# Performance work log

Measured on AMD Instinct MI355X. Metric: run time of the kernel, lower is better.

The kernel has to match this reference:

```python
import jax, jax.numpy as jnp
import numpy as np
import math

N_HEAD = 16

def _c(a):
    # stack real/imag -> complex64
    return jax.lax.complex(a[..., 0], a[..., 1])

def _rope_phasor(T, D, dtype=jnp.float32):
    inv_freq = 1.0 / (10000.0 ** (jnp.arange(D, dtype=dtype) / D))
    t = jnp.arange(T, dtype=dtype)
    freqs = jnp.outer(t, inv_freq)  # [T, D]
    return jax.lax.complex(jnp.cos(freqs), jnp.sin(freqs))

def setup_inputs() -> dict:
    key = jax.random.key(0)
    ks = jax.random.split(key, 9)
    B, T, C = 2, 1024, 1024
    s = 0.02
    return {
        "x":  jax.random.normal(ks[0], (B, T, C, 2), jnp.float32),
        "wq": jax.random.normal(ks[1], (C, C, 2), jnp.float32) * s,
        "bq": jax.random.normal(ks[2], (C, 2), jnp.float32) * s,
        "wk": jax.random.normal(ks[3], (C, C, 2), jnp.float32) * s,
        "bk": jax.random.normal(ks[4], (C, 2), jnp.float32) * s,
        "wv": jax.random.normal(ks[5], (C, C, 2), jnp.float32) * s,
        "bv": jax.random.normal(ks[6], (C, 2), jnp.float32) * s,
        "wo": jax.random.normal(ks[7], (C, C, 2), jnp.float32) * s,
        "bo": jax.random.normal(ks[8], (C, 2), jnp.float32) * s,
    }

def reference(x, wq, bq, wk, bk, wv, bv, wo, bo):
    B, T, C, _ = x.shape
    H = N_HEAD
    D = C // H
    xc = _c(x)
    # complex linear projections: y = x @ W^T + b
    q = xc @ _c(wq).T + _c(bq)
    k = xc @ _c(wk).T + _c(bk)
    v = xc @ _c(wv).T + _c(bv)
    # [B, T, C] -> [B, H, T, D]
    q = q.reshape(B, T, H, D).transpose(0, 2, 1, 3)
    k = k.reshape(B, T, H, D).transpose(0, 2, 1, 3)
    v = v.reshape(B, T, H, D).transpose(0, 2, 1, 3)
    # complex RoPE phasor multiply
    ph = _rope_phasor(T, D)[None, None]  # [1,1,T,D]
    q = q * ph
    k = k * ph
    # complex QK^H, scaled
    score = jnp.einsum('bhtd,bhsd->bhts', q, jnp.conj(k)) / math.sqrt(D)
    # softmax over magnitude, then real-valued complex weights
    attn = jax.nn.softmax(jnp.abs(score), axis=-1)
    attn_c = jax.lax.complex(attn, jnp.zeros_like(attn))
    out = jnp.einsum('bhts,bhsd->bhtd', attn_c, v)
    out = out.transpose(0, 2, 1, 3).reshape(B, T, C)
    out = out @ _c(wo).T + _c(bo)
    # return real/imag stacked for a real-valued harness
    return jnp.stack([out.real, out.imag], axis=-1)
```

## Files before the change

### kernel.cpp

```cpp
#include <hip/hip_runtime.h>
#include <math.h>

#define T_SEQ  1024
#define C_DIM  1024
#define NH_    16
#define H_DIM  64
#define SCL    (0.125f * 1.4426950408889634f)

typedef __bf16 bf16;
typedef __bf16 bf16x4 __attribute__((ext_vector_type(4)));
typedef __bf16 bf16x8 __attribute__((ext_vector_type(8)));
typedef float  f32x4  __attribute__((ext_vector_type(4)));

#define MFMA16(a, b, c) __builtin_amdgcn_mfma_f32_16x16x32_bf16(a, b, c, 0, 0, 0)

#define GLOAD_LDS16(g, l) __builtin_amdgcn_global_load_lds( \
    (const __attribute__((address_space(1))) void*)(g),     \
    (__attribute__((address_space(3))) void*)(l), 16, 0, 0)

__device__ __forceinline__ bf16x8 neg8(bf16x8 x) {
    union { bf16x8 v; unsigned int u[4]; } t;
    t.v = x;
    t.u[0] ^= 0x80008000u; t.u[1] ^= 0x80008000u;
    t.u[2] ^= 0x80008000u; t.u[3] ^= 0x80008000u;
    return t.v;
}

__device__ __forceinline__ bf16x8 frag_sw(const bf16* plane, int row, int chunk) {
    int c = chunk ^ (row & 7);
    return *(const bf16x8*)&plane[row * 64 + c * 8];
}
__device__ __forceinline__ bf16x8 frag_sw4(const bf16* plane, int row, int chunk) {
    int c = chunk ^ (row & 3);
    return *(const bf16x8*)&plane[row * 32 + c * 8];
}

__global__ __launch_bounds__(256)
void split_all(const float* __restrict__ x,  const float* __restrict__ wq,
               const float* __restrict__ wk, const float* __restrict__ wv,
               const float* __restrict__ wo,
               bf16* Xr, bf16* Xi, bf16* Wqr, bf16* Wqi, bf16* Wkr, bf16* Wki,
               bf16* Wvr, bf16* Wvi, bf16* Wor, bf16* Woi,
               float* __restrict__ rope)
{
    int z = blockIdx.y;
    if (z == 5) {
        if (blockIdx.x >= 256) return;
        int idx = blockIdx.x * 256 + threadIdx.x;
        int tp = idx >> 6, d = idx & 63;
        float invf = exp2f((float)d * -0.2076205059304601f);
        float fr = (float)tp * invf;
        float sn, cs; sincosf(fr, &sn, &cs);
        *(float2*)&rope[(size_t)idx * 2] = make_float2(cs, sn);
        return;
    }
    if (z > 0 && blockIdx.x >= 1024) return;
    const float* in; bf16 *pr, *pi;
    if      (z == 0) { in = x;  pr = Xr;  pi = Xi;  }
    else if (z == 1) { in = wq; pr = Wqr; pi = Wqi; }
    else if (z == 2) { in = wk; pr = Wkr; pi = Wki; }
    else if (z == 3) { in = wv; pr = Wvr; pi = Wvi; }
    else             { in = wo; pr = Wor; pi = Woi; }
    int idx = (blockIdx.x * 256 + threadIdx.x) * 4;
    float4 v0 = *(const float4*)(in + (size_t)idx * 2);
    float4 v1 = *(const float4*)(in + (size_t)idx * 2 + 4);
    bf16x4 r, im;
    r[0] = (bf16)v0.x; r[1] = (bf16)v0.z; r[2] = (bf16)v1.x; r[3] = (bf16)v1.z;
    im[0] = (bf16)v0.y; im[1] = (bf16)v0.w; im[2] = (bf16)v1.y; im[3] = (bf16)v1.w;
    *(bf16x4*)(pr + idx) = r;
    *(bf16x4*)(pi + idx) = im;
}

__device__ __forceinline__ void cgemm128(
    bf16* __restrict__ smem,
    const bf16* __restrict__ Ar, const bf16* __restrict__ Ai,
    const bf16* __restrict__ Br, const bf16* __restrict__ Bi,
    const float* __restrict__ bias, const float* __restrict__ rope,
    bf16* __restrict__ Yr, bf16* __restrict__ Yi, int m0, int n0, int mode)
{
    const int t = threadIdx.x, lane = t & 63, wave = t >> 6;
    const int wm = (wave >> 1) * 64, wn = (wave & 1) * 32;
    const int lm = lane & 15, quad = lane >> 4;
    const int s_lr = lane >> 3, s_c = (lane & 7) ^ s_lr;

    f32x4 accr[4][2], acci[4][2];
#pragma unroll
    for (int i = 0; i < 4; i++)
#pragma unroll
        for (int j = 0; j < 2; j++) { accr[i][j] = (f32x4)0.f; acci[i][j] = (f32x4)0.f; }

    for (int k0 = 0; k0 < C_DIM; k0 += 64) {
#pragma unroll
        for (int j = 0; j < 12; j++) {
            int c = wave + 4 * j;
            const bf16* src; bf16* dst;
            if (c < 16)      {             src = Ar + (size_t)(m0 + c * 8 + s_lr) * C_DIM + k0 + s_c * 8; dst = smem + c * 512; }
            else if (c < 32) { int u = c - 16; src = Ai + (size_t)(m0 + u * 8 + s_lr) * C_DIM + k0 + s_c * 8; dst = smem + 8192 + u * 512; }
            else if (c < 40) { int u = c - 32; src = Br + (size_t)(n0 + u * 8 + s_lr) * C_DIM + k0 + s_c * 8; dst = smem + 16384 + u * 512; }
            else             { int u = c - 40; src = Bi + (size_t)(n0 + u * 8 + s_lr) * C_DIM + k0 + s_c * 8; dst = smem + 20480 + u * 512; }
            GLOAD_LDS16(src, dst);
        }
        __syncthreads();

#pragma unroll
        for (int kh = 0; kh < 2; kh++) {
            bf16x8 ar[4], ai_[4], br_[2], bi_[2], bn_[2];
#pragma unroll
            for (int i = 0; i < 4; i++) {
                ar[i]  = frag_sw(smem,        wm + i * 16 + lm, kh * 4 + quad);
                ai_[i] = frag_sw(smem + 8192, wm + i * 16 + lm, kh * 4 + quad);
            }
#pragma unroll
            for (int j = 0; j < 2; j++) {
                br_[j] = frag_sw(smem + 16384, wn + j * 16 + lm, kh * 4 + quad);
                bi_[j] = frag_sw(smem + 20480, wn + j * 16 + lm, kh * 4 + quad);
                bn_[j] = neg8(bi_[j]);
            }
#pragma unroll
            for (int i = 0; i < 4; i++)
#pragma unroll
                for (int j = 0; j < 2; j++) {
                    accr[i][j] = MFMA16(ar[i],  br_[j], accr[i][j]);
                    accr[i][j] = MFMA16(ai_[i], bn_[j], accr[i][j]);
                    acci[i][j] = MFMA16(ar[i],  bi_[j], acci[i][j]);
                    acci[i][j] = MFMA16(ai_[i], br_[j], acci[i][j]);
                }
        }
        __syncthreads();
    }

    const int h = n0 >> 6, bb = m0 >> 10, tbase = m0 & (T_SEQ - 1);

    if (mode == 1) {
#pragma unroll
        for (int i = 0; i < 4; i++)
#pragma unroll
            for (int j = 0; j < 2; j++) {
                int d = wn + j * 16 + lm;
                float2 bv = *(const float2*)&bias[2 * (n0 + d)];
#pragma unroll
                for (int r = 0; r < 4; r++) {
                    int tpos = tbase + wm + i * 16 + quad * 4 + r;
                    float2 ph = *(const float2*)&rope[((size_t)tpos * H_DIM + d) * 2];
                    float yr = accr[i][j][r] + bv.x;
                    float yi = acci[i][j][r] + bv.y;
                    accr[i][j][r] = yr * ph.x - yi * ph.y;
                    acci[i][j][r] = yr * ph.y + yi * ph.x;
                }
            }
        bf16* dsts[2] = { Yr, Yi };
#pragma unroll
        for (int pass = 0; pass < 2; pass++) {
            __syncthreads();
#pragma unroll
            for (int i = 0; i < 4; i++)
#pragma unroll
                for (int j = 0; j < 2; j++)
#pragma unroll
                    for (int r = 0; r < 4; r++)
                        smem[(wm + i * 16 + quad * 4 + r) * 72 + wn + j * 16 + lm] =
                            (bf16)(pass ? acci[i][j][r] : accr[i][j][r]);
            __syncthreads();
            bf16* dst = dsts[pass] + ((size_t)(bb * NH_ + h) * T_SEQ + tbase) * H_DIM;
#pragma unroll
            for (int p = 0; p < 4; p++) {
                int ch = t + 256 * p;
                int row = ch >> 3, o = (ch & 7) * 8;
                *(bf16x8*)&dst[row * H_DIM + o] = *(const bf16x8*)&smem[row * 72 + o];
            }
        }
    } else {
        bf16* dsts[2] = { Yr, Yi };
#pragma unroll
        for (int pass = 0; pass < 2; pass++) {
            __syncthreads();
#pragma unroll
            for (int i = 0; i < 4; i++)
#pragma unroll
                for (int j = 0; j < 2; j++) {
                    int d = wn + j * 16 + lm;
                    float2 bv = *(const float2*)&bias[2 * (n0 + d)];
                    float bb2 = pass ? bv.y : bv.x;
                    bf16x4 pk;
#pragma unroll
                    for (int r = 0; r < 4; r++)
                        pk[r] = (bf16)((pass ? acci[i][j][r] : accr[i][j][r]) + bb2);
                    *(bf16x4*)&smem[d * 136 + wm + i * 16 + quad * 4] = pk;
                }
            __syncthreads();
            bf16* dst = dsts[pass] + ((size_t)(bb * NH_ + h) * H_DIM) * T_SEQ + tbase;
#pragma unroll
            for (int p = 0; p < 4; p++) {
                int ch = t + 256 * p;
                int row = ch >> 4, o = (ch & 15) * 8;
                *(bf16x8*)&dst[(size_t)row * T_SEQ + o] = *(const bf16x8*)&smem[row * 136 + o];
            }
        }
    }
}

__global__ __launch_bounds__(256, 3)
void qkv_gemm(const bf16* __restrict__ Xr, const bf16* __restrict__ Xi,
              const bf16* __restrict__ Wqr, const bf16* __restrict__ Wqi,
              const bf16* __restrict__ Wkr, const bf16* __restrict__ Wki,
              const bf16* __restrict__ Wvr, const bf16* __restrict__ Wvi,
              const float* __restrict__ bq, const float* __restrict__ bk,
              const float* __restrict__ bv, const float* __restrict__ rope,
              bf16* Qr, bf16* Qi, bf16* Kr, bf16* Ki, bf16* Vr, bf16* Vi)
{
    __shared__ __attribute__((aligned(16))) bf16 smem[24576];
    int m0 = blockIdx.y * 128, n0 = blockIdx.x * 64;
    const bf16 *Br, *Bi; const float* bias; bf16 *Yr, *Yi; int mode;
    if (blockIdx.z == 0)      { Br = Wqr; Bi = Wqi; bias = bq; Yr = Qr; Yi = Qi; mode = 1; }
    else if (blockIdx.z == 1) { Br = Wkr; Bi = Wki; bias = bk; Yr = Kr; Yi = Ki; mode = 1; }
    else                      { Br = Wvr; Bi = Wvi; bias = bv; Yr = Vr; Yi = Vi; mode = 2; }
    cgemm128(smem, Xr, Xi, Br, Bi, bias, rope, Yr, Yi, m0, n0, mode);
}

__global__ __launch_bounds__(256, 4)
void out_gemm(const bf16* __restrict__ Ar, const bf16* __restrict__ Ai,
              const bf16* __restrict__ Br, const bf16* __restrict__ Bi,
              const float* __restrict__ bias, float* __restrict__ Y)
{
    __shared__ __attribute__((aligned(16))) bf16 sm[16384];
    const int t = threadIdx.x, lane = t & 63, wave = t >> 6;
    const int lm = lane & 15, quad = lane >> 4;
    const int s_lr = lane >> 3, s_c = (lane & 7) ^ s_lr;
    const int wm = (wave >> 1) * 32, wn = (wave & 1) * 32;
    const int m0 = blockIdx.y * 64, n0 = blockIdx.x * 64;

    f32x4 accr[2][2], acci[2][2];
#pragma unroll
    for (int i = 0; i < 2; i++)
#pragma unroll
        for (int j = 0; j < 2; j++) { accr[i][j] = (f32x4)0.f; acci[i][j] = (f32x4)0.f; }

    for (int k0 = 0; k0 < C_DIM; k0 += 64) {
#pragma unroll
        for (int j = 0; j < 8; j++) {
            int c = wave + 4 * j;
            const bf16* src; bf16* dst;
            if (c < 8)       {             src = Ar + (size_t)(m0 + c * 8 + s_lr) * C_DIM + k0 + s_c * 8; dst = sm + c * 512; }
            else if (c < 16) { int u = c - 8;  src = Ai + (size_t)(m0 + u * 8 + s_lr) * C_DIM + k0 + s_c * 8; dst = sm + 4096 + u * 512; }
            else if (c < 24) { int u = c - 16; src = Br + (size_t)(n0 + u * 8 + s_lr) * C_DIM + k0 + s_c * 8; dst = sm + 8192 + u * 512; }
            else             { int u = c - 24; src = Bi + (size_t)(n0 + u * 8 + s_lr) * C_DIM + k0 + s_c * 8; dst = sm + 12288 + u * 512; }
            GLOAD_LDS16(src, dst);
        }
        __syncthreads();
#pragma unroll
        for (int kh = 0; kh < 2; kh++) {
            bf16x8 ar[2], ai_[2], br_[2], bi_[2], bn_[2];
#pragma unroll
            for (int i = 0; i < 2; i++) {
                ar[i]  = frag_sw(sm,        wm + i * 16 + lm, kh * 4 + quad);
                ai_[i] = frag_sw(sm + 4096, wm + i * 16 + lm, kh * 4 + quad);
            }
#pragma unroll
            for (int j = 0; j < 2; j++) {
                br_[j] = frag_sw(sm + 8192,  wn + j * 16 + lm, kh * 4 + quad);
                bi_[j] = frag_sw(sm + 12288, wn + j * 16 + lm, kh * 4 + quad);
                bn_[j] = neg8(bi_[j]);
            }
#pragma unroll
            for (int i = 0; i < 2; i++)
#pragma unroll
                for (int j = 0; j < 2; j++) {
                    accr[i][j] = MFMA16(ar[i],  br_[j], accr[i][j]);
                    accr[i][j] = MFMA16(ai_[i], bn_[j], accr[i][j]);
                    acci[i][j] = MFMA16(ar[i],  bi_[j], acci[i][j]);
                    acci[i][j] = MFMA16(ai_[i], br_[j], acci[i][j]);
                }
        }
        __syncthreads();
    }
#pragma unroll
    for (int i = 0; i < 2; i++)
#pragma unroll
        for (int j = 0; j < 2; j++) {
            int n = n0 + wn + j * 16 + lm;
            float2 bv = *(const float2*)&bias[2 * n];
#pragma unroll
            for (int r = 0; r < 4; r++) {
                int m = m0 + wm + i * 16 + quad * 4 + r;
                *(float2*)&Y[((size_t)m * C_DIM + n) * 2] =
                    make_float2(accr[i][j][r] + bv.x, acci[i][j][r] + bv.y);
            }
        }
}

__global__ __launch_bounds__(512, 4)
void attn_mfma(const bf16* __restrict__ Qpr, const bf16* __restrict__ Qpi,
               const bf16* __restrict__ Kpr, const bf16* __restrict__ Kpi,
               const bf16* __restrict__ Vtr, const bf16* __restrict__ Vti,
               bf16* __restrict__ ABr, bf16* __restrict__ ABi)
{
    __shared__ __attribute__((aligned(16))) bf16 smem[24576];
    const int t = threadIdx.x, lane = t & 63, w = t >> 6;
    const int qg = w & 3, sh = w >> 2;
    const int lm = lane & 15, quad = lane >> 4;
    const int q0 = blockIdx.x * 64;
    const int h = blockIdx.y, b = blockIdx.z;
    const size_t hb = (size_t)(b * NH_ + h) * T_SEQ * H_DIM;
    const int s_lr = lane >> 3, s_c = (lane & 7) ^ s_lr;
    const int lr4 = lane >> 2, sc4 = ((lane & 3) ^ (lr4 & 3)) * 8;

    {
        const bf16* gq = (sh == 0 ? Qpr : Qpi) + hb + (size_t)q0 * H_DIM;
        bf16* lq = smem + sh * 4096;
#pragma unroll
        for (int j = 0; j < 2; j++) {
            int cc = qg * 2 + j;
            GLOAD_LDS16(gq + (cc * 8 + s_lr) * H_DIM + s_c * 8, lq + cc * 512);
        }
    }
    __syncthreads();

    bf16x8 qfr[2], qfi[2], nqfr[2];
#pragma unroll
    for (int kh = 0; kh < 2; kh++) {
        qfr[kh]  = frag_sw(smem,        qg * 16 + lm, kh * 4 + quad);
        qfi[kh]  = frag_sw(smem + 4096, qg * 16 + lm, kh * 4 + quad);
        nqfr[kh] = neg8(qfr[kh]);
    }

    bf16* Ks_r = smem + 8192 + sh * 8192;
    bf16* Ks_i = Ks_r + 2048;
    bf16* Vs_r = Ks_r + 4096;
    bf16* Vs_i = Ks_r + 6144;
    bf16* Pl   = smem;
    const int prow = sh * 64 + qg * 16 + lm;

    f32x4 Or[4], Oi[4];
#pragma unroll
    for (int nt = 0; nt < 4; nt++) { Or[nt] = (f32x4)0.f; Oi[nt] = (f32x4)0.f; }
    float mold = 0.f, lsum = 0.f;

    for (int it = 0; it < 16; it++) {
        const int s0 = it * 32 + sh * 512;
        __syncthreads();
        {
            if (qg < 2) {
                const bf16* gsrc = (qg == 0 ? Kpr : Kpi) + hb + (size_t)s0 * H_DIM;
                bf16* ldst = (qg == 0) ? Ks_r : Ks_i;
#pragma unroll
                for (int cc = 0; cc < 4; cc++)
                    GLOAD_LDS16(gsrc + (cc * 8 + s_lr) * H_DIM + s_c * 8, ldst + cc * 512);
            } else {
                const bf16* gsrc = (qg == 2 ? Vtr : Vti) + hb + s0;
                bf16* ldst = (qg == 2) ? Vs_r : Vs_i;
#pragma unroll
                for (int cc = 0; cc < 4; cc++)
                    GLOAD_LDS16(gsrc + (size_t)(cc * 16 + lr4) * T_SEQ + sc4, ldst + cc * 512);
            }
        }
        __syncthreads();

        float sc[2][4];
#pragma unroll
        for (int ct = 0; ct < 2; ct++) {
            f32x4 sre = (f32x4)0.f, sim = (f32x4)0.f;
#pragma unroll
            for (int kh = 0; kh < 2; kh++) {
                bf16x8 kr = frag_sw(Ks_r, ct * 16 + lm, kh * 4 + quad);
                bf16x8 ki = frag_sw(Ks_i, ct * 16 + lm, kh * 4 + quad);
                sre = MFMA16(kr, qfr[kh],  sre);
                sre = MFMA16(ki, qfi[kh],  sre);
                sim = MFMA16(kr, qfi[kh],  sim);
                sim = MFMA16(ki, nqfr[kh], sim);
            }
#pragma unroll
            for (int r = 0; r < 4; r++)
                sc[ct][r] = sqrtf(sre[r] * sre[r] + sim[r] * sim[r]) * SCL;
        }

        float mx = sc[0][0];
#pragma unroll
        for (int ct = 0; ct < 2; ct++)
#pragma unroll
            for (int r = 0; r < 4; r++) mx = fmaxf(mx, sc[ct][r]);
        mx = fmaxf(mx, __shfl_xor(mx, 16));
        mx = fmaxf(mx, __shfl_xor(mx, 32));
        float mnew = fmaxf(mold, mx);
        float alpha = exp2f(mold - mnew);
        float ps = 0.f;
#pragma unroll
        for (int ct = 0; ct < 2; ct++) {
            bf16x4 pk;
#pragma unroll
            for (int r = 0; r < 4; r++) {
                float p = exp2f(sc[ct][r] - mnew);
                ps += p;
                pk[r] = (bf16)p;
            }
            *(bf16x4*)&Pl[prow * 40 + ct * 16 + quad * 4] = pk;
        }
        ps += __shfl_xor(ps, 16);
        ps += __shfl_xor(ps, 32);
        lsum = lsum * alpha + ps;
        mold = mnew;

        float aO[4];
#pragma unroll
        for (int r = 0; r < 4; r++)
            aO[r] = __shfl(alpha, (quad << 4) + quad * 4 + r, 64);
#pragma unroll
        for (int nt = 0; nt < 4; nt++)
#pragma unroll
            for (int r = 0; r < 4; r++) { Or[nt][r] *= aO[r]; Oi[nt][r] *= aO[r]; }

        bf16x8 pf = *(const bf16x8*)&Pl[prow * 40 + quad * 8];
#pragma unroll
        for (int nt = 0; nt < 4; nt++) {
            Or[nt] = MFMA16(pf, frag_sw4(Vs_r, nt * 16 + lm, quad), Or[nt]);
            Oi[nt] = MFMA16(pf, frag_sw4(Vs_i, nt * 16 + lm, quad), Oi[nt]);
        }
    }

    float* Of = (float*)(smem + 8192);
    float* ml = (float*)smem;
    __syncthreads();
    if (sh == 1) {
#pragma unroll
        for (int nt = 0; nt < 4; nt++)
#pragma unroll
            for (int r = 0; r < 4; r++) {
                Of[((qg * 2 + 0) * 16 + quad * 4 + r) * 64 + nt * 16 + lm] = Or[nt][r];
                Of[((qg * 2 + 1) * 16 + quad * 4 + r) * 64 + nt * 16 + lm] = Oi[nt][r];
            }
        if (quad == 0) *(float2*)&ml[(qg * 16 + lm) * 2] = make_float2(mold, lsum);
    }
    __syncthreads();
    if (sh == 0) {
        float2 m2 = *(const float2*)&ml[(qg * 16 + lm) * 2];
        float mn = fmaxf(mold, m2.x);
        float a1 = exp2f(mold - mn), a2 = exp2f(m2.x - mn);
        lsum = a1 * lsum + a2 * m2.y;
        float a1r[4], a2r[4], linv[4];
        float lv = 1.f / lsum;
#pragma unroll
        for (int r = 0; r < 4; r++) {
            int src = (quad << 4) + quad * 4 + r;
            a1r[r]  = __shfl(a1, src, 64);
            a2r[r]  = __shfl(a2, src, 64);
            linv[r] = __shfl(lv, src, 64);
        }
        size_t mbase = (size_t)(b * T_SEQ + q0 + qg * 16 + quad * 4) * C_DIM;
        int colb = h * H_DIM + lm;
#pragma unroll
        for (int nt = 0; nt < 4; nt++)
#pragma unroll
            for (int r = 0; r < 4; r++) {
                float orv = a1r[r] * Or[nt][r] +
                            a2r[r] * Of[((qg * 2 + 0) * 16 + quad * 4 + r) * 64 + nt * 16 + lm];
                float oiv = a1r[r] * Oi[nt][r] +
                            a2r[r] * Of[((qg * 2 + 1) * 16 + quad * 4 + r) * 64 + nt * 16 + lm];
                size_t o = mbase + (size_t)r * C_DIM + colb + nt * 16;
                ABr[o] = (bf16)(orv * linv[r]);
                ABi[o] = (bf16)(oiv * linv[r]);
            }
    }
}

extern "C" void kernel_launch(void* const* d_in, const int* in_sizes, int n_in,
                              void* d_out, int out_size, void* d_ws, size_t ws_size,
                              hipStream_t stream) {
    const float* x  = (const float*)d_in[0];
    const float* wq = (const float*)d_in[1];
    const float* bq = (const float*)d_in[2];
    const float* wk = (const float*)d_in[3];
    const float* bk = (const float*)d_in[4];
    const float* wv = (const float*)d_in[5];
    const float* bv = (const float*)d_in[6];
    const float* wo = (const float*)d_in[7];
    const float* bo = (const float*)d_in[8];

    float* rope = (float*)d_ws;
    bf16* w = (bf16*)(rope + 131072);
    const size_t MSZ = (size_t)2048 * 1024;
    const size_t WSZ = (size_t)1024 * 1024;
    const size_t PSZ = (size_t)2 * NH_ * T_SEQ * H_DIM;

    bf16 *Xr = w, *Xi = Xr + MSZ;
    bf16 *Wqr = Xi + MSZ,  *Wqi = Wqr + WSZ;
    bf16 *Wkr = Wqi + WSZ, *Wki = Wkr + WSZ;
    bf16 *Wvr = Wki + WSZ, *Wvi = Wvr + WSZ;
    bf16 *Wor = Wvi + WSZ, *Woi = Wor + WSZ;
    bf16 *Qr = Woi + WSZ, *Qi = Qr + PSZ;
    bf16 *Kr = Qi + PSZ,  *Ki = Kr + PSZ;
    bf16 *Vr = Ki + PSZ,  *Vi = Vr + PSZ;
    bf16 *ABr = Vi + PSZ, *ABi = ABr + MSZ;

    split_all<<<dim3(2048, 6), 256, 0, stream>>>(x, wq, wk, wv, wo,
        Xr, Xi, Wqr, Wqi, Wkr, Wki, Wvr, Wvi, Wor, Woi, rope);

    qkv_gemm<<<dim3(16, 16, 3), 256, 0, stream>>>(
        Xr, Xi, Wqr, Wqi, Wkr, Wki, Wvr, Wvi, bq, bk, bv, rope,
        Qr, Qi, Kr, Ki, Vr, Vi);

    attn_mfma<<<dim3(16, 16, 2), 512, 0, stream>>>(
        Qr, Qi, Kr, Ki, Vr, Vi, ABr, ABi);

    out_gemm<<<dim3(16, 32), 256, 0, stream>>>(ABr, ABi, Wor, Woi, bo, (float*)d_out);
}
```

Before: 238.0 us.

## Double-buffer K/V tiles in attention, drop running max, shuffle P in registers

```diff
diff --git a/kernel.cpp b/kernel.cpp
--- a/kernel.cpp
+++ b/kernel.cpp
@@ -54,21 +54,23 @@
         *(float2*)&rope[(size_t)idx * 2] = make_float2(cs, sn);
         return;
     }
-    if (z > 0 && blockIdx.x >= 1024) return;
+    if (z > 0 && blockIdx.x >= 512) return;
     const float* in; bf16 *pr, *pi;
     if      (z == 0) { in = x;  pr = Xr;  pi = Xi;  }
     else if (z == 1) { in = wq; pr = Wqr; pi = Wqi; }
     else if (z == 2) { in = wk; pr = Wkr; pi = Wki; }
     else if (z == 3) { in = wv; pr = Wvr; pi = Wvi; }
     else             { in = wo; pr = Wor; pi = Woi; }
-    int idx = (blockIdx.x * 256 + threadIdx.x) * 4;
-    float4 v0 = *(const float4*)(in + (size_t)idx * 2);
-    float4 v1 = *(const float4*)(in + (size_t)idx * 2 + 4);
-    bf16x4 r, im;
-    r[0] = (bf16)v0.x; r[1] = (bf16)v0.z; r[2] = (bf16)v1.x; r[3] = (bf16)v1.z;
-    im[0] = (bf16)v0.y; im[1] = (bf16)v0.w; im[2] = (bf16)v1.y; im[3] = (bf16)v1.w;
-    *(bf16x4*)(pr + idx) = r;
-    *(bf16x4*)(pi + idx) = im;
+    int idx = (blockIdx.x * 256 + threadIdx.x) * 8;
+    bf16x8 r, im;
+#pragma unroll
+    for (int j = 0; j < 4; j++) {
+        float4 v = *(const float4*)(in + (size_t)idx * 2 + j * 4);
+        r[2*j]   = (bf16)v.x; im[2*j]   = (bf16)v.y;
+        r[2*j+1] = (bf16)v.z; im[2*j+1] = (bf16)v.w;
+    }
+    *(bf16x8*)(pr + idx) = r;
+    *(bf16x8*)(pi + idx) = im;
 }
 
 __device__ __forceinline__ void cgemm128(
@@ -294,7 +296,7 @@
                const bf16* __restrict__ Vtr, const bf16* __restrict__ Vti,
                bf16* __restrict__ ABr, bf16* __restrict__ ABi)
 {
-    __shared__ __attribute__((aligned(16))) bf16 smem[24576];
+    __shared__ __attribute__((aligned(16))) bf16 smem[32768];
     const int t = threadIdx.x, lane = t & 63, w = t >> 6;
     const int qg = w & 3, sh = w >> 2;
     const int lm = lane & 15, quad = lane >> 4;
@@ -305,8 +307,8 @@
     const int lr4 = lane >> 2, sc4 = ((lane & 3) ^ (lr4 & 3)) * 8;
 
     {
-        const bf16* gq = (sh == 0 ? Qpr : Qpi) + hb + (size_t)q0 * H_DIM;
-        bf16* lq = smem + sh * 4096;
+        const bf16* gq = (sh ? Qpi : Qpr) + hb + (size_t)q0 * H_DIM;
+        bf16* lq = smem + 16384 + sh * 4096;
 #pragma unroll
         for (int j = 0; j < 2; j++) {
             int cc = qg * 2 + j;
@@ -318,142 +320,135 @@
     bf16x8 qfr[2], qfi[2], nqfr[2];
 #pragma unroll
     for (int kh = 0; kh < 2; kh++) {
-        qfr[kh]  = frag_sw(smem,        qg * 16 + lm, kh * 4 + quad);
-        qfi[kh]  = frag_sw(smem + 4096, qg * 16 + lm, kh * 4 + quad);
+        qfr[kh]  = frag_sw(smem + 16384, qg * 16 + lm, kh * 4 + quad);
+        qfi[kh]  = frag_sw(smem + 20480, qg * 16 + lm, kh * 4 + quad);
         nqfr[kh] = neg8(qfr[kh]);
     }
 
-    bf16* Ks_r = smem + 8192 + sh * 8192;
-    bf16* Ks_i = Ks_r + 2048;
-    bf16* Vs_r = Ks_r + 4096;
-    bf16* Vs_i = Ks_r + 6144;
-    bf16* Pl   = smem;
-    const int prow = sh * 64 + qg * 16 + lm;
+#pragma unroll
+    for (int pre = 0; pre < 1; pre++) {
+        const int S = sh * 512;
+        bf16* bd = smem + sh * 8192;
+        if (qg < 2) {
+            const bf16* g = (qg ? Kpi : Kpr) + hb + (size_t)S * H_DIM;
+            bf16* d = bd + (qg ? 2048 : 0);
+#pragma unroll
+            for (int cc = 0; cc < 4; cc++)
+                GLOAD_LDS16(g + (cc * 8 + s_lr) * H_DIM + s_c * 8, d + cc * 512);
+        } else {
+            const bf16* g = (qg == 2 ? Vtr : Vti) + hb + S;
+            bf16* d = bd + (qg == 2 ? 4096 : 6144);
+#pragma unroll
+            for (int cc = 0; cc < 4; cc++)
+                GLOAD_LDS16(g + (size_t)(cc * 16 + lr4) * T_SEQ + sc4, d + cc * 512);
+        }
+    }
 
     f32x4 Or[4], Oi[4];
 #pragma unroll
     for (int nt = 0; nt < 4; nt++) { Or[nt] = (f32x4)0.f; Oi[nt] = (f32x4)0.f; }
-    float mold = 0.f, lsum = 0.f;
+    float lsum = 0.f;
+    const int idxA = (((2 * quad) & 3) * 16 + lm) * 4;
+    const int idxB = idxA + 64;
+    const bool hisel = quad >= 2;
 
     for (int it = 0; it < 16; it++) {
-        const int s0 = it * 32 + sh * 512;
         __syncthreads();
-        {
+        if (it < 15) {
+            const int S = (it + 1) * 32 + sh * 512;
+            bf16* bd = smem + ((it + 1) & 1) * 16384 + sh * 8192;
             if (qg < 2) {
-                const bf16* gsrc = (qg == 0 ? Kpr : Kpi) + hb + (size_t)s0 * H_DIM;
-                bf16* ldst = (qg == 0) ? Ks_r : Ks_i;
+                const bf16* g = (qg ? Kpi : Kpr) + hb + (size_t)S * H_DIM;
+                bf16* d = bd + (qg ? 2048 : 0);
 #pragma unroll
                 for (int cc = 0; cc < 4; cc++)
-                    GLOAD_LDS16(gsrc + (cc * 8 + s_lr) * H_DIM + s_c * 8, ldst + cc * 512);
+                    GLOAD_LDS16(g + (cc * 8 + s_lr) * H_DIM + s_c * 8, d + cc * 512);
             } else {
-                const bf16* gsrc = (qg == 2 ? Vtr : Vti) + hb + s0;
-                bf16* ldst = (qg == 2) ? Vs_r : Vs_i;
+                const bf16* g = (qg == 2 ? Vtr : Vti) + hb + S;
+                bf16* d = bd + (qg == 2 ? 4096 : 6144);
 #pragma unroll
                 for (int cc = 0; cc < 4; cc++)
-                    GLOAD_LDS16(gsrc + (size_t)(cc * 16 + lr4) * T_SEQ + sc4, ldst + cc * 512);
-            }
-        }
-        __syncthreads();
-
-        float sc[2][4];
+                    GLOAD_LDS16(g + (size_t)(cc * 16 + lr4) * T_SEQ + sc4, d + cc * 512);
+            }
+        }
+        const bf16* buf = smem + (it & 1) * 16384 + sh * 8192;
+
+        union { unsigned int u[2]; bf16 b[4]; } pk[2];
 #pragma unroll
         for (int ct = 0; ct < 2; ct++) {
             f32x4 sre = (f32x4)0.f, sim = (f32x4)0.f;
 #pragma unroll
             for (int kh = 0; kh < 2; kh++) {
-                bf16x8 kr = frag_sw(Ks_r, ct * 16 + lm, kh * 4 + quad);
-                bf16x8 ki = frag_sw(Ks_i, ct * 16 + lm, kh * 4 + quad);
+                bf16x8 kr = frag_sw(buf,        ct * 16 + lm, kh * 4 + quad);
+                bf16x8 ki = frag_sw(buf + 2048, ct * 16 + lm, kh * 4 + quad);
                 sre = MFMA16(kr, qfr[kh],  sre);
                 sre = MFMA16(ki, qfi[kh],  sre);
                 sim = MFMA16(kr, qfi[kh],  sim);
                 sim = MFMA16(ki, nqfr[kh], sim);
             }
 #pragma unroll
-            for (int r = 0; r < 4; r++)
-                sc[ct][r] = sqrtf(sre[r] * sre[r] + sim[r] * sim[r]) * SCL;
-        }
-
-        float mx = sc[0][0];
-#pragma unroll
-        for (int ct = 0; ct < 2; ct++)
-#pragma unroll
-            for (int r = 0; r < 4; r++) mx = fmaxf(mx, sc[ct][r]);
-        mx = fmaxf(mx, __shfl_xor(mx, 16));
-        mx = fmaxf(mx, __shfl_xor(mx, 32));
-        float mnew = fmaxf(mold, mx);
-        float alpha = exp2f(mold - mnew);
-        float ps = 0.f;
-#pragma unroll
-        for (int ct = 0; ct < 2; ct++) {
-            bf16x4 pk;
-#pragma unroll
             for (int r = 0; r < 4; r++) {
-                float p = exp2f(sc[ct][r] - mnew);
-                ps += p;
-                pk[r] = (bf16)p;
-            }
-            *(bf16x4*)&Pl[prow * 40 + ct * 16 + quad * 4] = pk;
-        }
-        ps += __shfl_xor(ps, 16);
-        ps += __shfl_xor(ps, 32);
-        lsum = lsum * alpha + ps;
-        mold = mnew;
-
-        float aO[4];
-#pragma unroll
-        for (int r = 0; r < 4; r++)
-            aO[r] = __shfl(alpha, (quad << 4) + quad * 4 + r, 64);
+                float p = exp2f(sqrtf(sre[r] * sre[r] + sim[r] * sim[r]) * SCL);
+                lsum += p;
+                pk[ct].b[r] = (bf16)p;
+            }
+        }
+
+        union { unsigned int u[4]; bf16x8 v; } pf;
+        {
+            int a0 = __builtin_amdgcn_ds_bpermute(idxA, (int)pk[0].u[0]);
+            int a1 = __builtin_amdgcn_ds_bpermute(idxA, (int)pk[1].u[0]);
+            int b0 = __builtin_amdgcn_ds_bpermute(idxA, (int)pk[0].u[1]);
+            int b1 = __builtin_amdgcn_ds_bpermute(idxA, (int)pk[1].u[1]);
+            int c0 = __builtin_amdgcn_ds_bpermute(idxB, (int)pk[0].u[0]);
+            int c1 = __builtin_amdgcn_ds_bpermute(idxB, (int)pk[1].u[0]);
+            int d0 = __builtin_amdgcn_ds_bpermute(idxB, (int)pk[0].u[1]);
+            int d1 = __builtin_amdgcn_ds_bpermute(idxB, (int)pk[1].u[1]);
+            pf.u[0] = (unsigned int)(hisel ? a1 : a0);
+            pf.u[1] = (unsigned int)(hisel ? b1 : b0);
+            pf.u[2] = (unsigned int)(hisel ? c1 : c0);
+            pf.u[3] = (unsigned int)(hisel ? d1 : d0);
+        }
+
+#pragma unroll
+        for (int nt = 0; nt < 4; nt++) {
+            Or[nt] = MFMA16(pf.v, frag_sw4(buf + 4096, nt * 16 + lm, quad), Or[nt]);
+            Oi[nt] = MFMA16(pf.v, frag_sw4(buf + 6144, nt * 16 + lm, quad), Oi[nt]);
+        }
+    }
+
+    lsum += __shfl_xor(lsum, 16);
+    lsum += __shfl_xor(lsum, 32);
+
+    __syncthreads();
+    float* Of  = (float*)smem;
+    float* lsc = Of + 128 * 66;
+    if (sh == 1) {
 #pragma unroll
         for (int nt = 0; nt < 4; nt++)
 #pragma unroll
-            for (int r = 0; r < 4; r++) { Or[nt][r] *= aO[r]; Oi[nt][r] *= aO[r]; }
-
-        bf16x8 pf = *(const bf16x8*)&Pl[prow * 40 + quad * 8];
-#pragma unroll
-        for (int nt = 0; nt < 4; nt++) {
-            Or[nt] = MFMA16(pf, frag_sw4(Vs_r, nt * 16 + lm, quad), Or[nt]);
-            Oi[nt] = MFMA16(pf, frag_sw4(Vs_i, nt * 16 + lm, quad), Oi[nt]);
-        }
-    }
-
-    float* Of = (float*)(smem + 8192);
-    float* ml = (float*)smem;
-    __syncthreads();
-    if (sh == 1) {
-#pragma unroll
-        for (int nt = 0; nt < 4; nt++)
-#pragma unroll
             for (int r = 0; r < 4; r++) {
-                Of[((qg * 2 + 0) * 16 + quad * 4 + r) * 64 + nt * 16 + lm] = Or[nt][r];
-                Of[((qg * 2 + 1) * 16 + quad * 4 + r) * 64 + nt * 16 + lm] = Oi[nt][r];
-            }
-        if (quad == 0) *(float2*)&ml[(qg * 16 + lm) * 2] = make_float2(mold, lsum);
+                Of[((qg * 2 + 0) * 16 + quad * 4 + r) * 66 + nt * 16 + lm] = Or[nt][r];
+                Of[((qg * 2 + 1) * 16 + quad * 4 + r) * 66 + nt * 16 + lm] = Oi[nt][r];
+            }
+        if (quad == 0) lsc[qg * 16 + lm] = lsum;
     }
     __syncthreads();
     if (sh == 0) {
-        float2 m2 = *(const float2*)&ml[(qg * 16 + lm) * 2];
-        float mn = fmaxf(mold, m2.x);
-        float a1 = exp2f(mold - mn), a2 = exp2f(m2.x - mn);
-        lsum = a1 * lsum + a2 * m2.y;
-        float a1r[4], a2r[4], linv[4];
-        float lv = 1.f / lsum;
-#pragma unroll
-        for (int r = 0; r < 4; r++) {
-            int src = (quad << 4) + quad * 4 + r;
-            a1r[r]  = __shfl(a1, src, 64);
-            a2r[r]  = __shfl(a2, src, 64);
-            linv[r] = __shfl(lv, src, 64);
-        }
+        float ltot = lsum + lsc[qg * 16 + lm];
+        float lv = 1.f / ltot;
+        float linv[4];
+#pragma unroll
+        for (int r = 0; r < 4; r++)
+            linv[r] = __shfl(lv, (quad << 4) + quad * 4 + r, 64);
         size_t mbase = (size_t)(b * T_SEQ + q0 + qg * 16 + quad * 4) * C_DIM;
         int colb = h * H_DIM + lm;
 #pragma unroll
         for (int nt = 0; nt < 4; nt++)
 #pragma unroll
             for (int r = 0; r < 4; r++) {
-                float orv = a1r[r] * Or[nt][r] +
-                            a2r[r] * Of[((qg * 2 + 0) * 16 + quad * 4 + r) * 64 + nt * 16 + lm];
-                float oiv = a1r[r] * Oi[nt][r] +
-                            a2r[r] * Of[((qg * 2 + 1) * 16 + quad * 4 + r) * 64 + nt * 16 + lm];
+                float orv = Or[nt][r] + Of[((qg * 2 + 0) * 16 + quad * 4 + r) * 66 + nt * 16 + lm];
+                float oiv = Oi[nt][r] + Of[((qg * 2 + 1) * 16 + quad * 4 + r) * 66 + nt * 16 + lm];
                 size_t o = mbase + (size_t)r * C_DIM + colb + nt * 16;
                 ABr[o] = (bf16)(orv * linv[r]);
                 ABi[o] = (bf16)(oiv * linv[r]);
@@ -490,7 +485,7 @@
     bf16 *Vr = Ki + PSZ,  *Vi = Vr + PSZ;
     bf16 *ABr = Vi + PSZ, *ABi = ABr + MSZ;
 
-    split_all<<<dim3(2048, 6), 256, 0, stream>>>(x, wq, wk, wv, wo,
+    split_all<<<dim3(1024, 6), 256, 0, stream>>>(x, wq, wk, wv, wo,
         Xr, Xi, Wqr, Wqi, Wkr, Wki, Wvr, Wvi, Wor, Woi, rope);
 
     qkv_gemm<<<dim3(16, 16, 3), 256, 0, stream>>>(
```

Measured after the change: 217.0 us. 8.8% less time.
